# Performance work log

Hardware: AMD Instinct MI355X
Metric: run time of the kernel (lower is better)

Reference implementation:

```python
import jax, jax.numpy as jnp
import numpy as np

N_NODES = 100000
IN_CH = 128
HID = 128   # 2 * out_channels
OUT = 64    # out_channels
N_EDGES = 1000000


def _glorot(key, shape):
    lim = np.sqrt(6.0 / (shape[0] + shape[1]))
    return jax.random.uniform(key, shape, jnp.float32, -lim, lim)


def setup_inputs() -> dict:
    key = jax.random.key(0)
    ks = jax.random.split(key, 8)
    x = jax.random.normal(ks[0], (N_NODES, IN_CH), jnp.float32)
    edge_index = jax.random.randint(ks[1], (2, N_EDGES), 0, N_NODES, jnp.int64)
    return {
        "x": x,
        "edge_index": edge_index,
        # conv1: in -> 2*out
        "W1_l": _glorot(ks[2], (IN_CH, HID)),
        "W1_r": _glorot(ks[3], (IN_CH, HID)),
        "b1": jnp.zeros((HID,), jnp.float32),
        # conv_mu: 2*out -> out
        "Wmu_l": _glorot(ks[4], (HID, OUT)),
        "Wmu_r": _glorot(ks[5], (HID, OUT)),
        "bmu": jnp.zeros((OUT,), jnp.float32),
        # conv_logstd: 2*out -> out
        "Wls_l": _glorot(ks[6], (HID, OUT)),
        "Wls_r": _glorot(ks[7], (HID, OUT)),
        "bls": jnp.zeros((OUT,), jnp.float32),
    }


def _sage_conv(x, src, dst, W_l, W_r, b, n_nodes):
    # mean-aggregate neighbor features: messages flow src -> dst (PyG source_to_target)
    agg = jax.ops.segment_sum(x[src], dst, num_segments=n_nodes)          # [N, d]
    deg = jax.ops.segment_sum(jnp.ones(src.shape, x.dtype), dst, num_segments=n_nodes)
    agg = agg / jnp.maximum(deg, 1.0)[:, None]
    return agg @ W_l + x @ W_r + b


def reference(x, edge_index, W1_l, W1_r, b1, Wmu_l, Wmu_r, bmu, Wls_l, Wls_r, bls):
    src, dst = edge_index[0], edge_index[1]
    n = x.shape[0]
    h = jax.nn.relu(_sage_conv(x, src, dst, W1_l, W1_r, b1, n))
    mu = _sage_conv(h, src, dst, Wmu_l, Wmu_r, bmu, n)
    logstd = _sage_conv(h, src, dst, Wls_l, Wls_r, bls, n)
    return (mu, logstd)
```

## Files before the change

### kernel.cpp

```cpp
#include <hip/hip_runtime.h>

#define NN 100000
#define IC 128
#define OC 64
#define NE 1000000

#define NBUCK 256
#define BN 392
#define RCAP 4608
#define EPB 2048
#define CAPA 24
#define GPAD 16
#define LDW 136
#define BINA_GRID 489
#define CVT_BLOCKS 6250

typedef __attribute__((ext_vector_type(8))) short short8;
typedef __attribute__((ext_vector_type(4))) float f32x4;

static __device__ __forceinline__ float b2f(unsigned short u) {
    unsigned v = ((unsigned)u) << 16;
    float f;
    __builtin_memcpy(&f, &v, 4);
    return f;
}
static __device__ __forceinline__ unsigned short f2b(float f) {
    unsigned u;
    __builtin_memcpy(&u, &f, 4);
    u += 0x7fff + ((u >> 16) & 1);
    return (unsigned short)(u >> 16);
}

#if defined(__has_builtin)
#if __has_builtin(__builtin_amdgcn_cvt_pk_fp8_f32) && __has_builtin(__builtin_amdgcn_cvt_pk_f32_fp8)
#define HW_FP8 1
#endif
#endif

static __device__ __forceinline__ unsigned f2q1(float f) {
    unsigned u;
    __builtin_memcpy(&u, &f, 4);
    unsigned s = (u >> 24) & 0x80u;
    unsigned a = u & 0x7FFFFFFFu;
    if (a < 0x3C000000u) return s;
    if (a < 0x3C800000u) return s | 0x08u;
    if (a >= 0x43E00000u) return s | 0x7Eu;
    a += 0x7FFFFu + ((a >> 20) & 1u);
    unsigned e = (a >> 23) - 120u;
    unsigned m = (a >> 20) & 7u;
    unsigned c = (e << 3) | m;
    if (c > 0x7Eu) c = 0x7Eu;
    return s | c;
}
static __device__ __forceinline__ float q1f(unsigned q) {
    unsigned em = q & 0x7Fu;
    unsigned s = (q & 0x80u) << 24;
    unsigned u = (em >= 8u) ? (s | (((em >> 3) + 120u) << 23) | ((em & 7u) << 20)) : s;
    float f;
    __builtin_memcpy(&f, &u, 4);
    return f;
}

static __device__ __forceinline__ unsigned pack4_fp8(float a, float b, float c, float d) {
#ifdef HW_FP8
    int r = __builtin_amdgcn_cvt_pk_fp8_f32(a, b, 0, false);
    r = __builtin_amdgcn_cvt_pk_fp8_f32(c, d, r, true);
    return (unsigned)r;
#else
    return f2q1(a) | (f2q1(b) << 8) | (f2q1(c) << 16) | (f2q1(d) << 24);
#endif
}
static __device__ __forceinline__ void dec4(unsigned w, float* o) {
#ifdef HW_FP8
    auto p0 = __builtin_amdgcn_cvt_pk_f32_fp8((int)w, false);
    auto p1 = __builtin_amdgcn_cvt_pk_f32_fp8((int)w, true);
    o[0] = p0[0]; o[1] = p0[1]; o[2] = p1[0]; o[3] = p1[1];
#else
#pragma unroll
    for (int q = 0; q < 4; ++q) o[q] = q1f((w >> (8 * q)) & 0xFFu);
#endif
}

__device__ __forceinline__ void binA_body(int blk, int t,
                                          const int* __restrict__ src,
                                          const int* __restrict__ dst,
                                          int* __restrict__ gcur,
                                          unsigned* __restrict__ bins,
                                          unsigned (*buf)[CAPA], int* lcnt, int* goff) {
    lcnt[t] = 0;
    __syncthreads();
    const int e0 = blk * EPB;
#pragma unroll
    for (int q = 0; q < EPB / 256; ++q) {
        int e = e0 + q * 256 + t;
        if (e < NE) {
            int d = dst[e];
            int s = src[e];
            int b = d / BN;
            unsigned packed = ((unsigned)(d - b * BN) << 17) | (unsigned)s;
            int idx = atomicAdd(&lcnt[b], 1);
            if (idx < CAPA) {
                buf[b][idx] = packed;
            } else {
                int g = atomicAdd(&gcur[b * GPAD], 1);
                if (g < RCAP) bins[(size_t)b * RCAP + g] = packed;
            }
        }
    }
    __syncthreads();
    int c = lcnt[t];
    if (c > CAPA) c = CAPA;
    if (c > 0) goff[t] = atomicAdd(&gcur[t * GPAD], c);
    __syncthreads();
    const int wid = t >> 6, lane = t & 63;
    for (int b = wid * 64; b < wid * 64 + 64; ++b) {
        int cb = lcnt[b];
        if (cb > CAPA) cb = CAPA;
        if (lane < cb) {
            int g = goff[b] + lane;
            if (g < RCAP) bins[(size_t)b * RCAP + g] = buf[b][lane];
        }
    }
}

__global__ __launch_bounds__(256) void k_front(
    const int* __restrict__ src, const int* __restrict__ dst,
    int* __restrict__ gcur, unsigned* __restrict__ bins,
    const float* __restrict__ x, unsigned short* __restrict__ xb,
    unsigned char* __restrict__ xq,
    const float* __restrict__ W1l, const float* __restrict__ W1r,
    const float* __restrict__ Wml, const float* __restrict__ Wmr,
    const float* __restrict__ Wsl, const float* __restrict__ Wsr,
    unsigned short* __restrict__ Wf1, unsigned short* __restrict__ Wf2) {
    __shared__ unsigned buf[NBUCK][CAPA];
    __shared__ int lcnt[NBUCK];
    __shared__ int goff[NBUCK];
    const int blk = blockIdx.x;
    const int tid = threadIdx.x;
    if (blk < BINA_GRID) {
        binA_body(blk, tid, src, dst, gcur, bins, buf, lcnt, goff);
    } else if (blk < BINA_GRID + CVT_BLOCKS) {
        int t = (blk - BINA_GRID) * 256 + tid;
        const float4* p = (const float4*)x + (size_t)t * 2;
        float4 f0 = p[0], f1 = p[1];
        short8 o;
        o[0] = (short)f2b(f0.x); o[1] = (short)f2b(f0.y);
        o[2] = (short)f2b(f0.z); o[3] = (short)f2b(f0.w);
        o[4] = (short)f2b(f1.x); o[5] = (short)f2b(f1.y);
        o[6] = (short)f2b(f1.z); o[7] = (short)f2b(f1.w);
        *((short8*)xb + t) = o;
        uint2 q;
        q.x = pack4_fp8(f0.x, f0.y, f0.z, f0.w);
        q.y = pack4_fp8(f1.x, f1.y, f1.z, f1.w);
        *((uint2*)xq + t) = q;
    } else {
        int t = (blk - BINA_GRID - CVT_BLOCKS) * 256 + tid;
        if (t >= 2 * 4096) return;
        const int layer = t >> 12;
        const int f = t & 4095;
        const int lane = f & 63;
        const int nt = (f >> 6) & 7;
        const int ks = f >> 9;
        const int col = nt * 16 + (lane & 15);
        const int kb = ks * 32 + ((lane >> 4) << 3);
        short8 o;
#pragma unroll
        for (int e = 0; e < 8; ++e) {
            const int k = kb + e;
            float v;
            if (layer == 0) {
                v = (k < 128) ? W1l[k * 128 + col] : W1r[(k - 128) * 128 + col];
            } else {
                if (col < OC) v = (k < 128) ? Wml[k * OC + col] : Wmr[(k - 128) * OC + col];
                else {
                    int c2 = col - OC;
                    v = (k < 128) ? Wsl[k * OC + c2] : Wsr[(k - 128) * OC + c2];
                }
            }
            o[e] = (short)f2b(v);
        }
        unsigned short* W = (layer == 0) ? Wf1 : Wf2;
        *(short8*)(W + (size_t)f * 8) = o;
    }
}

__global__ __launch_bounds__(256) void k_binB(const int* __restrict__ gcur,
                                              const unsigned* __restrict__ bins,
                                              int* __restrict__ row_ptr,
                                              int* __restrict__ csr,
                                              int* __restrict__ order) {
    __shared__ int lc[512];
    __shared__ int rk[512];
    __shared__ int tsum[256];
    __shared__ int dh[64];
    __shared__ int seg[RCAP];
    __shared__ int sh_bs;
    const int b = blockIdx.x;
    const int t = threadIdx.x;
    const int base = b * BN;
    const int nloc = (NN - base < BN) ? (NN - base) : BN;
    int v = gcur[t * GPAD];
    if (v > RCAP) v = RCAP;
    tsum[t] = v;
    __syncthreads();
    for (int off = 1; off < 256; off <<= 1) {
        int u = (t >= off) ? tsum[t - off] : 0;
        __syncthreads();
        tsum[t] += u;
        __syncthreads();
    }
    if (t == b) sh_bs = tsum[t] - v;
    if (b == 0 && t == 255) row_ptr[NN] = tsum[255];
    lc[t] = 0; lc[t + 256] = 0;
    rk[t] = 0; rk[t + 256] = 0;
    if (t < 64) dh[t] = 0;
    __syncthreads();
    int c = gcur[b * GPAD];
    if (c > RCAP) c = RCAP;
    const unsigned* mb = bins + (size_t)b * RCAP;
    for (int i = t; i < c; i += 256) atomicAdd(&lc[mb[i] >> 17], 1);
    __syncthreads();
    int l0 = lc[2 * t], l1 = lc[2 * t + 1];
    const int d0 = (l0 < 64) ? l0 : 63;
    const int d1 = (l1 < 64) ? l1 : 63;
    if (2 * t < nloc) atomicAdd(&dh[d0], 1);
    if (2 * t + 1 < nloc) atomicAdd(&dh[d1], 1);
    int s = l0 + l1;
    tsum[t] = s;
    __syncthreads();
    for (int off = 1; off < 256; off <<= 1) {
        int u = (t >= off) ? tsum[t - off] : 0;
        __syncthreads();
        tsum[t] += u;
        __syncthreads();
    }
    int run = tsum[t] - s;
    lc[2 * t] = run;
    lc[2 * t + 1] = run + l0;
    if (t < 64) {
        int dv = dh[t];
        int sc = dv;
        for (int off = 1; off < 64; off <<= 1) {
            int u = __shfl_up(sc, off, 64);
            if (t >= off) sc += u;
        }
        dh[t] = sc - dv;
    }
    __syncthreads();
    if (2 * t < nloc) { int p = atomicAdd(&dh[d0], 1); order[base + p] = base + 2 * t; }
    if (2 * t + 1 < nloc) { int p = atomicAdd(&dh[d1], 1); order[base + p] = base + 2 * t + 1; }
    const int bs = sh_bs;
    for (int i = t; i < nloc; i += 256) row_ptr[base + i] = bs + lc[i];
    for (int i = t; i < c; i += 256) {
        unsigned p = mb[i];
        int dl = p >> 17;
        int r = atomicAdd(&rk[dl], 1);
        seg[lc[dl] + r] = (int)(p & 0x1FFFFu);
    }
    __syncthreads();
    for (int i = t; i < c; i += 256) csr[bs + i] = seg[i];
}

template <int FP8>
__global__ __launch_bounds__(256) void k_agg(const unsigned short* __restrict__ feat,
                                             const unsigned char* __restrict__ featq,
                                             const int* __restrict__ row_ptr,
                                             const int* __restrict__ csr,
                                             const int* __restrict__ order,
                                             unsigned short* __restrict__ agg) {
    const int lane = threadIdx.x & 63;
    const int wid = threadIdx.x >> 6;
    if (FP8) {
        const int slot = lane >> 3;
        const int cl = lane & 7;
        const int idx = blockIdx.x * 32 + wid * 8 + slot;
        if (idx >= NN) return;
        const int node = order[idx];
        const int beg = row_ptr[node];
        const int end = row_ptr[node + 1];
        if (beg == end) {
            short8 z = {0, 0, 0, 0, 0, 0, 0, 0};
            *(short8*)(agg + (size_t)node * IC + cl * 16) = z;
            *(short8*)(agg + (size_t)node * IC + cl * 16 + 8) = z;
            return;
        }
        const int last = end - 1;
        float acc[16];
#pragma unroll
        for (int q = 0; q < 16; ++q) acc[q] = 0.f;
        int sidx[8];
#pragma unroll
        for (int u = 0; u < 8; ++u) {
            int jj = beg + u;
            sidx[u] = csr[(jj < last) ? jj : last];
        }
        for (int j = beg; j < end; j += 8) {
            uint4 v[8];
#pragma unroll
            for (int u = 0; u < 8; ++u)
                v[u] = *(const uint4*)(featq + (size_t)sidx[u] * IC + cl * 16);
            const int jn = j + 8;
            if (jn < end) {
#pragma unroll
                for (int u = 0; u < 8; ++u) {
                    int jj = jn + u;
                    sidx[u] = csr[(jj < last) ? jj : last];
                }
            }
#pragma unroll
            for (int u = 0; u < 8; ++u) {
                const bool ok = (j + u) < end;
                float d[16];
                dec4(v[u].x, d); dec4(v[u].y, d + 4);
                dec4(v[u].z, d + 8); dec4(v[u].w, d + 12);
#pragma unroll
                for (int q = 0; q < 16; ++q) acc[q] += ok ? d[q] : 0.f;
            }
        }
        float inv = 1.0f / (float)(end - beg);
        short8 o0, o1;
#pragma unroll
        for (int q = 0; q < 8; ++q) o0[q] = (short)f2b(acc[q] * inv);
#pragma unroll
        for (int q = 0; q < 8; ++q) o1[q] = (short)f2b(acc[8 + q] * inv);
        *(short8*)(agg + (size_t)node * IC + cl * 16) = o0;
        *(short8*)(agg + (size_t)node * IC + cl * 16 + 8) = o1;
    } else {
        const int slot = lane >> 4;
        const int cg = lane & 15;
        const int idx = blockIdx.x * 16 + wid * 4 + slot;
        if (idx >= NN) return;
        const int node = order[idx];
        const int beg = row_ptr[node];
        const int end = row_ptr[node + 1];
        if (beg == end) {
            short8 z = {0, 0, 0, 0, 0, 0, 0, 0};
            *(short8*)(agg + (size_t)node * IC + cg * 8) = z;
            return;
        }
        const int last = end - 1;
        float acc[8];
#pragma unroll
        for (int q = 0; q < 8; ++q) acc[q] = 0.f;
        int sidx[8];
#pragma unroll
        for (int u = 0; u < 8; ++u) {
            int jj = beg + u;
            sidx[u] = csr[(jj < last) ? jj : last];
        }
        for (int j = beg; j < end; j += 8) {
            short8 v[8];
#pragma unroll
            for (int u = 0; u < 8; ++u)
                v[u] = *(const short8*)(feat + (size_t)sidx[u] * IC + cg * 8);
            const int jn = j + 8;
            if (jn < end) {
#pragma unroll
                for (int u = 0; u < 8; ++u) {
                    int jj = jn + u;
                    sidx[u] = csr[(jj < last) ? jj : last];
                }
            }
#pragma unroll
            for (int u = 0; u < 8; ++u) {
                const bool ok = (j + u) < end;
#pragma unroll
                for (int q = 0; q < 8; ++q)
                    acc[q] += ok ? b2f((unsigned short)v[u][q]) : 0.f;
            }
        }
        float inv = 1.0f / (float)(end - beg);
        short8 o;
#pragma unroll
        for (int q = 0; q < 8; ++q) o[q] = (short)f2b(acc[q] * inv);
        *(short8*)(agg + (size_t)node * IC + cg * 8) = o;
    }
}

template <int MODE>
__global__ __launch_bounds__(256) void k_gemm(
    const unsigned short* __restrict__ Agg, const unsigned short* __restrict__ Xb,
    const unsigned short* __restrict__ Wf,
    const float* __restrict__ bias0, const float* __restrict__ bias1,
    unsigned short* __restrict__ hout, float* __restrict__ out_mu,
    float* __restrict__ out_ls) {
    const int lane = threadIdx.x & 63;
    const int wid = threadIdx.x >> 6;
    const int rowg = blockIdx.x * 128 + wid * 32;
    const int r16 = lane & 15;
    const int k8 = (lane >> 4) * 8;

    __shared__ unsigned short smem[MODE == 0 ? (4 * 32 * LDW) : 16384];
    short8* bsm = (short8*)smem;

    int rA[2];
#pragma unroll
    for (int m = 0; m < 2; ++m) {
        int r = rowg + m * 16 + r16;
        rA[m] = (r < NN) ? r : (NN - 1);
    }

    short8 aF[2][8];
#pragma unroll
    for (int ks = 0; ks < 4; ++ks) {
        aF[0][ks] = *(const short8*)(Agg + (size_t)rA[0] * IC + ks * 32 + k8);
        aF[1][ks] = *(const short8*)(Agg + (size_t)rA[1] * IC + ks * 32 + k8);
    }
#pragma unroll
    for (int ks = 0; ks < 4; ++ks) {
        aF[0][4 + ks] = *(const short8*)(Xb + (size_t)rA[0] * IC + ks * 32 + k8);
        aF[1][4 + ks] = *(const short8*)(Xb + (size_t)rA[1] * IC + ks * 32 + k8);
    }

    const short8* Wg = (const short8*)Wf;
#pragma unroll
    for (int i = 0; i < 8; ++i)
        bsm[i * 256 + threadIdx.x] = Wg[i * 256 + threadIdx.x];

#pragma unroll
    for (int ks = 0; ks < 8; ++ks)
        asm volatile("" :: "v"(aF[0][ks]), "v"(aF[1][ks]));

    __syncthreads();

    f32x4 acc[2][8];
#pragma unroll
    for (int m = 0; m < 2; ++m)
#pragma unroll
        for (int nt = 0; nt < 8; ++nt) acc[m][nt] = (f32x4){0.f, 0.f, 0.f, 0.f};

#pragma unroll
    for (int ks = 0; ks < 4; ++ks) {
        short8 bF[8];
#pragma unroll
        for (int nt = 0; nt < 8; ++nt) bF[nt] = bsm[(ks * 8 + nt) * 64 + lane];
#pragma unroll
        for (int nt = 0; nt < 8; ++nt) {
            acc[0][nt] = __builtin_amdgcn_mfma_f32_16x16x32_bf16(aF[0][ks], bF[nt], acc[0][nt], 0, 0, 0);
            acc[1][nt] = __builtin_amdgcn_mfma_f32_16x16x32_bf16(aF[1][ks], bF[nt], acc[1][nt], 0, 0, 0);
        }
    }
    __syncthreads();
#pragma unroll
    for (int i = 0; i < 8; ++i)
        bsm[i * 256 + threadIdx.x] = Wg[2048 + i * 256 + threadIdx.x];
    __syncthreads();
#pragma unroll
    for (int ks = 4; ks < 8; ++ks) {
        short8 bF[8];
#pragma unroll
        for (int nt = 0; nt < 8; ++nt) bF[nt] = bsm[((ks - 4) * 8 + nt) * 64 + lane];
#pragma unroll
        for (int nt = 0; nt < 8; ++nt) {
            acc[0][nt] = __builtin_amdgcn_mfma_f32_16x16x32_bf16(aF[0][ks], bF[nt], acc[0][nt], 0, 0, 0);
            acc[1][nt] = __builtin_amdgcn_mfma_f32_16x16x32_bf16(aF[1][ks], bF[nt], acc[1][nt], 0, 0, 0);
        }
    }

    const int rbase = (lane >> 4) * 4;
    if (MODE == 0) {
        __syncthreads();
        unsigned short* ws = smem + wid * 32 * LDW;
#pragma unroll
        for (int m = 0; m < 2; ++m) {
#pragma unroll
            for (int nt = 0; nt < 8; ++nt) {
                const int c = nt * 16 + r16;
                const float bv = bias0[c];
#pragma unroll
                for (int q = 0; q < 4; ++q) {
                    float v = fmaxf(acc[m][nt][q] + bv, 0.f);
                    ws[(m * 16 + rbase + q) * LDW + c] = f2b(v);
                }
            }
        }
        __syncthreads();
#pragma unroll
        for (int p = 0; p < 8; ++p) {
            const int rloc = p * 4 + (lane >> 4);
            const int row = rowg + rloc;
            if (row < NN) {
                short8 v = *(const short8*)&ws[rloc * LDW + r16 * 8];
                *(short8*)(hout + (size_t)row * IC + r16 * 8) = v;
            }
        }
    } else {
#pragma unroll
        for (int m = 0; m < 2; ++m) {
#pragma unroll
            for (int nt = 0; nt < 8; ++nt) {
                const int c = nt * 16 + r16;
                const float bv = (c < OC) ? bias0[c] : bias1[c - OC];
#pragma unroll
                for (int q = 0; q < 4; ++q) {
                    const int row = rowg + m * 16 + rbase + q;
                    if (row >= NN) continue;
                    float v = acc[m][nt][q] + bv;
                    if (c < OC) out_mu[(size_t)row * OC + c] = v;
                    else        out_ls[(size_t)row * OC + (c - OC)] = v;
                }
            }
        }
    }
}

extern "C" void kernel_launch(void* const* d_in, const int* in_sizes, int n_in,
                              void* d_out, int out_size, void* d_ws, size_t ws_size,
                              hipStream_t stream) {
    const float* x   = (const float*)d_in[0];
    const int*   ei  = (const int*)d_in[1];
    const float* W1l = (const float*)d_in[2];
    const float* W1r = (const float*)d_in[3];
    const float* b1  = (const float*)d_in[4];
    const float* Wml = (const float*)d_in[5];
    const float* Wmr = (const float*)d_in[6];
    const float* bm  = (const float*)d_in[7];
    const float* Wsl = (const float*)d_in[8];
    const float* Wsr = (const float*)d_in[9];
    const float* bs  = (const float*)d_in[10];

    const int* src = ei;
    const int* dst = ei + NE;

    char* w = (char*)d_ws;
    unsigned short* xb   = (unsigned short*)(w);
    unsigned short* hb   = (unsigned short*)(w + 25600000);
    unsigned short* aggb = (unsigned short*)(w + 51200000);
    unsigned short* Wf1  = (unsigned short*)(w + 76800000);
    unsigned short* Wf2  = (unsigned short*)(w + 76865536);
    int* row_ptr  = (int*)(w + 76931072);
    int* csr      = (int*)(w + 77331200);
    int* gcur     = (int*)(w + 81331200);
    unsigned* bins = (unsigned*)(w + 81347584);
    unsigned char* xq = (unsigned char*)(w + 86066176);
    int* order    = (int*)(w + 98866176);

    float* out_mu = (float*)d_out;
    float* out_ls = out_mu + (size_t)NN * OC;

    const int gemm_grid = (NN + 127) / 128;
    const int agg1_grid = (NN + 31) / 32;
    const int agg2_grid = (NN + 15) / 16;

    hipMemsetAsync(gcur, 0, NBUCK * GPAD * sizeof(int), stream);
    k_front<<<BINA_GRID + CVT_BLOCKS + 32, 256, 0, stream>>>(
        src, dst, gcur, bins, x, xb, xq, W1l, W1r, Wml, Wmr, Wsl, Wsr, Wf1, Wf2);
    k_binB<<<NBUCK, 256, 0, stream>>>(gcur, bins, row_ptr, csr, order);

    k_agg<1><<<agg1_grid, 256, 0, stream>>>(nullptr, xq, row_ptr, csr, order, aggb);
    k_gemm<0><<<gemm_grid, 256, 0, stream>>>(aggb, xb, Wf1, b1, nullptr,
                                             hb, nullptr, nullptr);

    k_agg<0><<<agg2_grid, 256, 0, stream>>>(hb, nullptr, row_ptr, csr, order, aggb);
    k_gemm<1><<<gemm_grid, 256, 0, stream>>>(aggb, hb, Wf2, bm, bs,
                                             nullptr, out_mu, out_ls);
}
```

Before: 164.9 us.

## Fuse neighbor aggregation into GEMM kernels via shared-memory staging

Measured after the change: 169.6 us. 1.03x slower.

```diff
diff --git a/kernel.cpp b/kernel.cpp
--- a/kernel.cpp
+++ b/kernel.cpp
@@ -261,206 +261,207 @@
     for (int i = t; i < c; i += 256) csr[bs + i] = seg[i];
 }
 
-template <int FP8>
-__global__ __launch_bounds__(256) void k_agg(const unsigned short* __restrict__ feat,
-                                             const unsigned char* __restrict__ featq,
-                                             const int* __restrict__ row_ptr,
-                                             const int* __restrict__ csr,
-                                             const int* __restrict__ order,
-                                             unsigned short* __restrict__ agg) {
-    const int lane = threadIdx.x & 63;
-    const int wid = threadIdx.x >> 6;
-    if (FP8) {
+template <int MODE>
+__global__ __launch_bounds__(256) void k_fgemm(
+    const unsigned char* __restrict__ gq, const unsigned short* __restrict__ gb,
+    const unsigned short* __restrict__ Xb, const unsigned short* __restrict__ Wf,
+    const float* __restrict__ bias0, const float* __restrict__ bias1,
+    const int* __restrict__ row_ptr, const int* __restrict__ csr,
+    const int* __restrict__ order,
+    unsigned short* __restrict__ hout, float* __restrict__ out_mu,
+    float* __restrict__ out_ls) {
+    const int tid = threadIdx.x;
+    const int lane = tid & 63;
+    const int wid = tid >> 6;
+    const int r16 = lane & 15;
+    const int k8 = (lane >> 4) * 8;
+    const int rowg = blockIdx.x * 128;
+
+    __shared__ short8 smemF[3104];
+    short8* aggF = smemF;
+    short8* bq = smemF + 2048;
+    int* sOrder = (int*)(smemF + 3072);
+
+    if (tid < 128) {
+        int idx = rowg + tid;
+        sOrder[tid] = (idx < NN) ? order[idx] : 0;
+    }
+    __syncthreads();
+
+    int rX[2];
+#pragma unroll
+    for (int m = 0; m < 2; ++m) rX[m] = sOrder[wid * 32 + m * 16 + r16];
+    short8 aFx[2][4];
+#pragma unroll
+    for (int ks = 0; ks < 4; ++ks) {
+        aFx[0][ks] = *(const short8*)(Xb + (size_t)rX[0] * IC + ks * 32 + k8);
+        aFx[1][ks] = *(const short8*)(Xb + (size_t)rX[1] * IC + ks * 32 + k8);
+    }
+
+    if (MODE == 0) {
         const int slot = lane >> 3;
         const int cl = lane & 7;
-        const int idx = blockIdx.x * 32 + wid * 8 + slot;
-        if (idx >= NN) return;
-        const int node = order[idx];
-        const int beg = row_ptr[node];
-        const int end = row_ptr[node + 1];
-        if (beg == end) {
-            short8 z = {0, 0, 0, 0, 0, 0, 0, 0};
-            *(short8*)(agg + (size_t)node * IC + cl * 16) = z;
-            *(short8*)(agg + (size_t)node * IC + cl * 16 + 8) = z;
-            return;
-        }
-        const int last = end - 1;
-        float acc[16];
-#pragma unroll
-        for (int q = 0; q < 16; ++q) acc[q] = 0.f;
-        int sidx[8];
-#pragma unroll
-        for (int u = 0; u < 8; ++u) {
-            int jj = beg + u;
-            sidx[u] = csr[(jj < last) ? jj : last];
-        }
-        for (int j = beg; j < end; j += 8) {
-            uint4 v[8];
-#pragma unroll
-            for (int u = 0; u < 8; ++u)
-                v[u] = *(const uint4*)(featq + (size_t)sidx[u] * IC + cl * 16);
-            const int jn = j + 8;
-            if (jn < end) {
+        const int ksw = cl >> 1, hi = cl & 1;
+#pragma unroll
+        for (int it = 0; it < 4; ++it) {
+            const int rl = it * 32 + wid * 8 + slot;
+            const int g = rl >> 4;
+            const int f1 = (g * 4 + ksw) * 64 + hi * 32 + (rl & 15);
+            const int gidx = rowg + rl;
+            const int node = sOrder[rl];
+            int beg = 0, end = 0;
+            if (gidx < NN) { beg = row_ptr[node]; end = row_ptr[node + 1]; }
+            if (beg == end) {
+                short8 z = {0, 0, 0, 0, 0, 0, 0, 0};
+                aggF[f1] = z;
+                aggF[f1 + 16] = z;
+                continue;
+            }
+            const int last = end - 1;
+            float acc[16];
+#pragma unroll
+            for (int q = 0; q < 16; ++q) acc[q] = 0.f;
+            int sidx[8];
+#pragma unroll
+            for (int u = 0; u < 8; ++u) {
+                int jj = beg + u;
+                sidx[u] = csr[(jj < last) ? jj : last];
+            }
+            for (int j = beg; j < end; j += 8) {
+                uint4 v[8];
+#pragma unroll
+                for (int u = 0; u < 8; ++u)
+                    v[u] = *(const uint4*)(gq + (size_t)sidx[u] * IC + cl * 16);
+                const int jn = j + 8;
+                if (jn < end) {
+#pragma unroll
+                    for (int u = 0; u < 8; ++u) {
+                        int jj = jn + u;
+                        sidx[u] = csr[(jj < last) ? jj : last];
+                    }
+                }
 #pragma unroll
                 for (int u = 0; u < 8; ++u) {
-                    int jj = jn + u;
-                    sidx[u] = csr[(jj < last) ? jj : last];
-                }
-            }
-#pragma unroll
-            for (int u = 0; u < 8; ++u) {
-                const bool ok = (j + u) < end;
-                float d[16];
-                dec4(v[u].x, d); dec4(v[u].y, d + 4);
-                dec4(v[u].z, d + 8); dec4(v[u].w, d + 12);
-#pragma unroll
-                for (int q = 0; q < 16; ++q) acc[q] += ok ? d[q] : 0.f;
-            }
-        }
-        float inv = 1.0f / (float)(end - beg);
-        short8 o0, o1;
-#pragma unroll
-        for (int q = 0; q < 8; ++q) o0[q] = (short)f2b(acc[q] * inv);
-#pragma unroll
-        for (int q = 0; q < 8; ++q) o1[q] = (short)f2b(acc[8 + q] * inv);
-        *(short8*)(agg + (size_t)node * IC + cl * 16) = o0;
-        *(short8*)(agg + (size_t)node * IC + cl * 16 + 8) = o1;
+                    const bool ok = (j + u) < end;
+                    float d[16];
+                    dec4(v[u].x, d); dec4(v[u].y, d + 4);
+                    dec4(v[u].z, d + 8); dec4(v[u].w, d + 12);
+#pragma unroll
+                    for (int q = 0; q < 16; ++q) acc[q] += ok ? d[q] : 0.f;
+                }
+            }
+            float inv = 1.0f / (float)(end - beg);
+            short8 o0, o1;
+#pragma unroll
+            for (int q = 0; q < 8; ++q) o0[q] = (short)f2b(acc[q] * inv);
+#pragma unroll
+            for (int q = 0; q < 8; ++q) o1[q] = (short)f2b(acc[8 + q] * inv);
+            aggF[f1] = o0;
+            aggF[f1 + 16] = o1;
+        }
     } else {
         const int slot = lane >> 4;
         const int cg = lane & 15;
-        const int idx = blockIdx.x * 16 + wid * 4 + slot;
-        if (idx >= NN) return;
-        const int node = order[idx];
-        const int beg = row_ptr[node];
-        const int end = row_ptr[node + 1];
-        if (beg == end) {
-            short8 z = {0, 0, 0, 0, 0, 0, 0, 0};
-            *(short8*)(agg + (size_t)node * IC + cg * 8) = z;
-            return;
-        }
-        const int last = end - 1;
-        float acc[8];
-#pragma unroll
-        for (int q = 0; q < 8; ++q) acc[q] = 0.f;
-        int sidx[8];
-#pragma unroll
-        for (int u = 0; u < 8; ++u) {
-            int jj = beg + u;
-            sidx[u] = csr[(jj < last) ? jj : last];
-        }
-        for (int j = beg; j < end; j += 8) {
-            short8 v[8];
-#pragma unroll
-            for (int u = 0; u < 8; ++u)
-                v[u] = *(const short8*)(feat + (size_t)sidx[u] * IC + cg * 8);
-            const int jn = j + 8;
-            if (jn < end) {
+        const int ksw = cg >> 2;
+        const int l16 = cg & 3;
+#pragma unroll
+        for (int it = 0; it < 8; ++it) {
+            const int rl = it * 16 + wid * 4 + slot;
+            const int g = rl >> 4;
+            const int f1 = (g * 4 + ksw) * 64 + l16 * 16 + (rl & 15);
+            const int gidx = rowg + rl;
+            const int node = sOrder[rl];
+            int beg = 0, end = 0;
+            if (gidx < NN) { beg = row_ptr[node]; end = row_ptr[node + 1]; }
+            if (beg == end) {
+                short8 z = {0, 0, 0, 0, 0, 0, 0, 0};
+                aggF[f1] = z;
+                continue;
+            }
+            const int last = end - 1;
+            float acc[8];
+#pragma unroll
+            for (int q = 0; q < 8; ++q) acc[q] = 0.f;
+            int sidx[8];
+#pragma unroll
+            for (int u = 0; u < 8; ++u) {
+                int jj = beg + u;
+                sidx[u] = csr[(jj < last) ? jj : last];
+            }
+            for (int j = beg; j < end; j += 8) {
+                short8 v[8];
+#pragma unroll
+                for (int u = 0; u < 8; ++u)
+                    v[u] = *(const short8*)(gb + (size_t)sidx[u] * IC + cg * 8);
+                const int jn = j + 8;
+                if (jn < end) {
+#pragma unroll
+                    for (int u = 0; u < 8; ++u) {
+                        int jj = jn + u;
+                        sidx[u] = csr[(jj < last) ? jj : last];
+                    }
+                }
 #pragma unroll
                 for (int u = 0; u < 8; ++u) {
-                    int jj = jn + u;
-                    sidx[u] = csr[(jj < last) ? jj : last];
-                }
-            }
-#pragma unroll
-            for (int u = 0; u < 8; ++u) {
-                const bool ok = (j + u) < end;
-#pragma unroll
-                for (int q = 0; q < 8; ++q)
-                    acc[q] += ok ? b2f((unsigned short)v[u][q]) : 0.f;
-            }
-        }
-        float inv = 1.0f / (float)(end - beg);
-        short8 o;
-#pragma unroll
-        for (int q = 0; q < 8; ++q) o[q] = (short)f2b(acc[q] * inv);
-        *(short8*)(agg + (size_t)node * IC + cg * 8) = o;
-    }
-}
-
-template <int MODE>
-__global__ __launch_bounds__(256) void k_gemm(
-    const unsigned short* __restrict__ Agg, const unsigned short* __restrict__ Xb,
-    const unsigned short* __restrict__ Wf,
-    const float* __restrict__ bias0, const float* __restrict__ bias1,
-    unsigned short* __restrict__ hout, float* __restrict__ out_mu,
-    float* __restrict__ out_ls) {
-    const int lane = threadIdx.x & 63;
-    const int wid = threadIdx.x >> 6;
-    const int rowg = blockIdx.x * 128 + wid * 32;
-    const int r16 = lane & 15;
-    const int k8 = (lane >> 4) * 8;
-
-    __shared__ unsigned short smem[MODE == 0 ? (4 * 32 * LDW) : 16384];
-    short8* bsm = (short8*)smem;
-
-    int rA[2];
-#pragma unroll
-    for (int m = 0; m < 2; ++m) {
-        int r = rowg + m * 16 + r16;
-        rA[m] = (r < NN) ? r : (NN - 1);
-    }
-
-    short8 aF[2][8];
+                    const bool ok = (j + u) < end;
+#pragma unroll
+                    for (int q = 0; q < 8; ++q)
+                        acc[q] += ok ? b2f((unsigned short)v[u][q]) : 0.f;
+                }
+            }
+            float inv = 1.0f / (float)(end - beg);
+            short8 o;
+#pragma unroll
+            for (int q = 0; q < 8; ++q) o[q] = (short)f2b(acc[q] * inv);
+            aggF[f1] = o;
+        }
+    }
+#pragma unroll
+    for (int ks = 0; ks < 4; ++ks)
+        asm volatile("" :: "v"(aFx[0][ks]), "v"(aFx[1][ks]));
+    __syncthreads();
+
+    short8 aFa[2][4];
 #pragma unroll
     for (int ks = 0; ks < 4; ++ks) {
-        aF[0][ks] = *(const short8*)(Agg + (size_t)rA[0] * IC + ks * 32 + k8);
-        aF[1][ks] = *(const short8*)(Agg + (size_t)rA[1] * IC + ks * 32 + k8);
-    }
-#pragma unroll
-    for (int ks = 0; ks < 4; ++ks) {
-        aF[0][4 + ks] = *(const short8*)(Xb + (size_t)rA[0] * IC + ks * 32 + k8);
-        aF[1][4 + ks] = *(const short8*)(Xb + (size_t)rA[1] * IC + ks * 32 + k8);
-    }
+        aFa[0][ks] = aggF[((wid * 2 + 0) * 4 + ks) * 64 + lane];
+        aFa[1][ks] = aggF[((wid * 2 + 1) * 4 + ks) * 64 + lane];
+    }
+
+    f32x4 acc[2][8];
+#pragma unroll
+    for (int m = 0; m < 2; ++m)
+#pragma unroll
+        for (int nt = 0; nt < 8; ++nt) acc[m][nt] = (f32x4){0.f, 0.f, 0.f, 0.f};
 
     const short8* Wg = (const short8*)Wf;
 #pragma unroll
-    for (int i = 0; i < 8; ++i)
-        bsm[i * 256 + threadIdx.x] = Wg[i * 256 + threadIdx.x];
-
-#pragma unroll
-    for (int ks = 0; ks < 8; ++ks)
-        asm volatile("" :: "v"(aF[0][ks]), "v"(aF[1][ks]));
-
-    __syncthreads();
-
-    f32x4 acc[2][8];
-#pragma unroll
-    for (int m = 0; m < 2; ++m)
-#pragma unroll
-        for (int nt = 0; nt < 8; ++nt) acc[m][nt] = (f32x4){0.f, 0.f, 0.f, 0.f};
-
-#pragma unroll
-    for (int ks = 0; ks < 4; ++ks) {
-        short8 bF[8];
-#pragma unroll
-        for (int nt = 0; nt < 8; ++nt) bF[nt] = bsm[(ks * 8 + nt) * 64 + lane];
-#pragma unroll
-        for (int nt = 0; nt < 8; ++nt) {
-            acc[0][nt] = __builtin_amdgcn_mfma_f32_16x16x32_bf16(aF[0][ks], bF[nt], acc[0][nt], 0, 0, 0);
-            acc[1][nt] = __builtin_amdgcn_mfma_f32_16x16x32_bf16(aF[1][ks], bF[nt], acc[1][nt], 0, 0, 0);
-        }
-    }
-    __syncthreads();
-#pragma unroll
-    for (int i = 0; i < 8; ++i)
-        bsm[i * 256 + threadIdx.x] = Wg[2048 + i * 256 + threadIdx.x];
-    __syncthreads();
-#pragma unroll
-    for (int ks = 4; ks < 8; ++ks) {
-        short8 bF[8];
-#pragma unroll
-        for (int nt = 0; nt < 8; ++nt) bF[nt] = bsm[((ks - 4) * 8 + nt) * 64 + lane];
-#pragma unroll
-        for (int nt = 0; nt < 8; ++nt) {
-            acc[0][nt] = __builtin_amdgcn_mfma_f32_16x16x32_bf16(aF[0][ks], bF[nt], acc[0][nt], 0, 0, 0);
-            acc[1][nt] = __builtin_amdgcn_mfma_f32_16x16x32_bf16(aF[1][ks], bF[nt], acc[1][nt], 0, 0, 0);
+    for (int ksq = 0; ksq < 4; ++ksq) {
+        __syncthreads();
+#pragma unroll
+        for (int i = 0; i < 4; ++i)
+            bq[i * 256 + tid] = Wg[ksq * 1024 + i * 256 + tid];
+        __syncthreads();
+#pragma unroll
+        for (int ksl = 0; ksl < 2; ++ksl) {
+            const int ks = ksq * 2 + ksl;
+            const short8 a0 = (ks < 4) ? aFa[0][ks] : aFx[0][ks - 4];
+            const short8 a1 = (ks < 4) ? aFa[1][ks] : aFx[1][ks - 4];
+            short8 bF[8];
+#pragma unroll
+            for (int nt = 0; nt < 8; ++nt) bF[nt] = bq[(ksl * 8 + nt) * 64 + lane];
+#pragma unroll
+            for (int nt = 0; nt < 8; ++nt) {
+                acc[0][nt] = __builtin_amdgcn_mfma_f32_16x16x32_bf16(a0, bF[nt], acc[0][nt], 0, 0, 0);
+                acc[1][nt] = __builtin_amdgcn_mfma_f32_16x16x32_bf16(a1, bF[nt], acc[1][nt], 0, 0, 0);
+            }
         }
     }
 
     const int rbase = (lane >> 4) * 4;
     if (MODE == 0) {
         __syncthreads();
-        unsigned short* ws = smem + wid * 32 * LDW;
+        unsigned short* ws = (unsigned short*)smemF + wid * 32 * LDW;
 #pragma unroll
         for (int m = 0; m < 2; ++m) {
 #pragma unroll
@@ -478,10 +479,11 @@
 #pragma unroll
         for (int p = 0; p < 8; ++p) {
             const int rloc = p * 4 + (lane >> 4);
-            const int row = rowg + rloc;
-            if (row < NN) {
+            const int rl = wid * 32 + rloc;
+            if (rowg + rl < NN) {
+                const int gr = sOrder[rl];
                 short8 v = *(const short8*)&ws[rloc * LDW + r16 * 8];
-                *(short8*)(hout + (size_t)row * IC + r16 * 8) = v;
+                *(short8*)(hout + (size_t)gr * IC + r16 * 8) = v;
             }
         }
     } else {
@@ -493,11 +495,12 @@
                 const float bv = (c < OC) ? bias0[c] : bias1[c - OC];
 #pragma unroll
                 for (int q = 0; q < 4; ++q) {
-                    const int row = rowg + m * 16 + rbase + q;
-                    if (row >= NN) continue;
+                    const int rl = wid * 32 + m * 16 + rbase + q;
+                    if (rowg + rl >= NN) continue;
+                    const int gr = sOrder[rl];
                     float v = acc[m][nt][q] + bv;
-                    if (c < OC) out_mu[(size_t)row * OC + c] = v;
-                    else        out_ls[(size_t)row * OC + (c - OC)] = v;
+                    if (c < OC) out_mu[(size_t)gr * OC + c] = v;
+                    else        out_ls[(size_t)gr * OC + (c - OC)] = v;
                 }
             }
         }
@@ -525,7 +528,6 @@
     char* w = (char*)d_ws;
     unsigned short* xb   = (unsigned short*)(w);
     unsigned short* hb   = (unsigned short*)(w + 25600000);
-    unsigned short* aggb = (unsigned short*)(w + 51200000);
     unsigned short* Wf1  = (unsigned short*)(w + 76800000);
     unsigned short* Wf2  = (unsigned short*)(w + 76865536);
     int* row_ptr  = (int*)(w + 76931072);
@@ -539,19 +541,17 @@
     float* out_ls = out_mu + (size_t)NN * OC;
 
     const int gemm_grid = (NN + 127) / 128;
-    const int agg1_grid = (NN + 31) / 32;
-    const int agg2_grid = (NN + 15) / 16;
 
     hipMemsetAsync(gcur, 0, NBUCK * GPAD * sizeof(int), stream);
     k_front<<<BINA_GRID + CVT_BLOCKS + 32, 256, 0, stream>>>(
         src, dst, gcur, bins, x, xb, xq, W1l, W1r, Wml, Wmr, Wsl, Wsr, Wf1, Wf2);
     k_binB<<<NBUCK, 256, 0, stream>>>(gcur, bins, row_ptr, csr, order);
 
-    k_agg<1><<<agg1_grid, 256, 0, stream>>>(nullptr, xq, row_ptr, csr, order, aggb);
-    k_gemm<0><<<gemm_grid, 256, 0, stream>>>(aggb, xb, Wf1, b1, nullptr,
-                                             hb, nullptr, nullptr);
-
-    k_agg<0><<<agg2_grid, 256, 0, stream>>>(hb, nullptr, row_ptr, csr, order, aggb);
-    k_gemm<1><<<gemm_grid, 256, 0, stream>>>(aggb, hb, Wf2, bm, bs,
-                                             nullptr, out_mu, out_ls);
-}
+    k_fgemm<0><<<gemm_grid, 256, 0, stream>>>(xq, nullptr, xb, Wf1, b1, nullptr,
+                                              row_ptr, csr, order,
+                                              hb, nullptr, nullptr);
+
+    k_fgemm<1><<<gemm_grid, 256, 0, stream>>>(nullptr, hb, hb, Wf2, bm, bs,
+                                              row_ptr, csr, order,
+                                              nullptr, out_mu, out_ls);
+}
```
